# Optimization experiments

Hardware: AMD Instinct MI355X
Metric: run time of the kernel (lower is better)

The kernel has to match this reference:

```python
import jax, jax.numpy as jnp
import numpy as np
import math

DIM = 1024
CHUNK = 64
B, S = 4, 4096

def setup_inputs() -> dict:
    key = jax.random.key(0)
    ks = jax.random.split(key, 16)
    d = DIM
    std = 1.0 / math.sqrt(d)
    def lin(k):
        k1, k2 = jax.random.split(k)
        return (jax.random.uniform(k1, (d, d), jnp.float32, -std, std),
                jax.random.uniform(k2, (d,), jnp.float32, -std, std))
    Wk, bk = lin(ks[0])
    Wv, bv = lin(ks[1])
    Wq, bq = lin(ks[2])
    Wkp, bkp = lin(ks[3])
    Wqp, bqp = lin(ks[4])
    Wo, bo = lin(ks[5])
    return {
        "x": jax.random.normal(ks[6], (B, S, d), jnp.float32),
        "Wk": Wk, "bk": bk, "Wv": Wv, "bv": bv, "Wq": Wq, "bq": bq,
        "Wkp": Wkp, "bkp": bkp, "Wqp": Wqp, "bqp": bqp,
        "phase_scale": jnp.full((d,), math.pi, jnp.float32),
        "ln_g": jnp.ones((d,), jnp.float32),
        "ln_b": jnp.zeros((d,), jnp.float32),
        "Wo": Wo, "bo": bo,
    }

def _linear(x, W, b):
    # torch nn.Linear: x @ W.T + b
    return jnp.einsum('bsd,ed->bse', x, W) + b

def _layernorm(x, g, b, eps=1e-5):
    mu = jnp.mean(x, axis=-1, keepdims=True)
    var = jnp.var(x, axis=-1, keepdims=True)
    return (x - mu) * jax.lax.rsqrt(var + eps) * g + b

def reference(x, Wk, bk, Wv, bv, Wq, bq, Wkp, bkp, Wqp, bqp,
              phase_scale, ln_g, ln_b, Wo, bo):
    batch, seq_len, dim = x.shape
    key = _linear(x, Wk, bk)
    value = _linear(x, Wv, bv)
    query = _linear(x, Wq, bq)
    key_phase = jnp.tanh(_linear(key, Wkp, bkp)) * phase_scale
    query_phase = jnp.tanh(_linear(query, Wqp, bqp)) * phase_scale
    bound_real = value * jnp.cos(key_phase)
    bound_imag = value * jnpp_sin(key_phase) if False else value * jnp.sin(key_phase)
    pad_len = (CHUNK - seq_len % CHUNK) % CHUNK
    if pad_len > 0:
        pad = ((0, 0), (0, pad_len), (0, 0))
        bound_real = jnp.pad(bound_real, pad)
        bound_imag = jnp.pad(bound_imag, pad)
        query_phase = jnp.pad(query_phase, pad)
    padded_len = bound_real.shape[1]
    nc = padded_len // CHUNK
    br = bound_real.reshape(batch, nc, CHUNK, dim)
    bi = bound_imag.reshape(batch, nc, CHUNK, dim)
    qp = query_phase.reshape(batch, nc, CHUNK, dim)
    mem_real = jnp.cumsum(br, axis=2)
    mem_imag = jnp.cumsum(bi, axis=2)
    retrieved = mem_real * jnp.cos(qp) + mem_imag * jnp.sin(qp)
    retrieved = retrieved.reshape(batch, padded_len, dim)[:, :seq_len]
    retrieved = retrieved / math.sqrt(dim)
    out = _linear(_layernorm(retrieved, ln_g, ln_b), Wo, bo)
    return x + out
```

## Files before the change

### kernel.cpp

```cpp
#include <hip/hip_runtime.h>
#include <math.h>

#define DIMD 1024
#define CHUNKLEN 64
#define NTOK 16384

#define TM 128
#define TN 128
#define BK 64

typedef __bf16 bf16x8 __attribute__((ext_vector_type(8)));
typedef float floatx4 __attribute__((ext_vector_type(4)));
typedef unsigned short ushort8v __attribute__((ext_vector_type(8)));

__device__ __forceinline__ float bf2f(unsigned short u) {
  union { unsigned int i; float f; } v; v.i = ((unsigned int)u) << 16; return v.f;
}
__device__ __forceinline__ unsigned short f2bf(float f) {
  union { float f; unsigned int i; } v; v.f = f;
  unsigned int r = v.i + 0x7FFFu + ((v.i >> 16) & 1u);
  return (unsigned short)(r >> 16);
}

__device__ __forceinline__ float tanh_fast(float v) {
  const float t = __expf(2.0f * v);
  return 1.0f - 2.0f * __builtin_amdgcn_rcpf(t + 1.0f);
}

__device__ __forceinline__ void async16(const unsigned short* g, unsigned short* l) {
  __builtin_amdgcn_global_load_lds(
      (const __attribute__((address_space(1))) unsigned int*)g,
      (__attribute__((address_space(3))) unsigned int*)l, 16, 0, 0);
}

__global__ __launch_bounds__(256) void cvt_all_kernel(
    const float* __restrict__ x,
    const float* __restrict__ w0, const float* __restrict__ w1,
    const float* __restrict__ w2, const float* __restrict__ w3,
    unsigned short* __restrict__ dx,
    unsigned short* __restrict__ d0, unsigned short* __restrict__ d1,
    unsigned short* __restrict__ d2, unsigned short* __restrict__ d3)
{
  const int b = blockIdx.x;
  const float* src; unsigned short* dst; long i;
  if (b < 16384) {
    src = x; dst = dx; i = (long)b * 256 + threadIdx.x;
  } else {
    const int r = b - 16384;
    const int s = r >> 10;
    src = s == 0 ? w0 : s == 1 ? w1 : s == 2 ? w2 : w3;
    dst = s == 0 ? d0 : s == 1 ? d1 : s == 2 ? d2 : d3;
    i = (long)(r & 1023) * 256 + threadIdx.x;
  }
  const float4 v = ((const float4*)src)[i];
  ushort4 o;
  o.x = f2bf(v.x); o.y = f2bf(v.y); o.z = f2bf(v.z); o.w = f2bf(v.w);
  ((ushort4*)dst)[i] = o;
}

__global__ __launch_bounds__(256) void transpose_cvt_kernel(
    const float* __restrict__ s0, const float* __restrict__ s1,
    unsigned short* __restrict__ q0, unsigned short* __restrict__ q1)
{
  __shared__ unsigned short tile[64][66];
  const float* src = blockIdx.z ? s1 : s0;
  unsigned short* dst = blockIdx.z ? q1 : q0;
  const int e0 = blockIdx.y * 64;
  const int k0 = blockIdx.x * 64;
  const int t  = threadIdx.x;
  const int tr = t >> 4;
  const int tc = t & 15;
#pragma unroll
  for (int p = 0; p < 4; ++p) {
    const int el = p * 16 + tr;
    const float4 v = *(const float4*)&src[(long)(e0 + el) * DIMD + k0 + tc * 4];
    tile[el][tc * 4 + 0] = f2bf(v.x);
    tile[el][tc * 4 + 1] = f2bf(v.y);
    tile[el][tc * 4 + 2] = f2bf(v.z);
    tile[el][tc * 4 + 3] = f2bf(v.w);
  }
  __syncthreads();
#pragma unroll
  for (int p = 0; p < 4; ++p) {
    const int kl = p * 16 + tr;
    ushort4 o;
    o.x = tile[tc * 4 + 0][kl];
    o.y = tile[tc * 4 + 1][kl];
    o.z = tile[tc * 4 + 2][kl];
    o.w = tile[tc * 4 + 3][kl];
    *(ushort4*)&dst[(long)(k0 + kl) * DIMD + e0 + tc * 4] = o;
  }
}

__global__ __launch_bounds__(256) void bias_comb_kernel(
    const float* __restrict__ Wkp, const float* __restrict__ bk,
    const float* __restrict__ bkp,
    const float* __restrict__ Wqp, const float* __restrict__ bq,
    const float* __restrict__ bqp,
    float* __restrict__ bkq, float* __restrict__ bqq)
{
  const int b = blockIdx.x;
  const int which = b >> 8;
  const int lane = threadIdx.x & 63;
  const int wid  = threadIdx.x >> 6;
  const int n = (b & 255) * 4 + wid;
  const float* W    = which ? Wqp : Wkp;
  const float* bvec = which ? bq  : bk;
  const float* badd = which ? bqp : bkp;
  float*       outp = which ? bqq : bkq;
  float s = 0.f;
#pragma unroll
  for (int i = 0; i < 16; ++i)
    s += W[(long)n * DIMD + lane + i * 64] * bvec[lane + i * 64];
#pragma unroll
  for (int o = 32; o > 0; o >>= 1) s += __shfl_xor(s, o, 64);
  if (lane == 0) outp[n] = s + badd[n];
}

template <int MODE>
__global__ __launch_bounds__(256) void gemm_bt_kernel(
    const unsigned short* __restrict__ A0, const unsigned short* __restrict__ A1,
    const unsigned short* __restrict__ W0, const unsigned short* __restrict__ W1,
    const unsigned short* __restrict__ W2,
    const float* __restrict__ b0, const float* __restrict__ b1,
    const float* __restrict__ b2,
    const float* __restrict__ aux,
    unsigned short* __restrict__ O0, unsigned short* __restrict__ O1,
    unsigned short* __restrict__ O2,
    float* __restrict__ Of, const float* __restrict__ resid)
{
  __shared__ unsigned short lsA[TM * BK];
  __shared__ unsigned short lsB[TN * BK];

  const int tid  = threadIdx.x;
  const int lane = tid & 63;
  const int wid  = tid >> 6;
  const long bm  = (long)blockIdx.y * TM;
  const long bng = (long)blockIdx.x * TN;

  const unsigned short* A = A0;
  const unsigned short* W = W0;
  const float* bias = b0;
  unsigned short* Ob = O0;
  long bn = bng;
  int seg = 0;
  if (MODE == 0) {
    seg = (int)(bng >> 10);
    bn = bng & 1023;
    W    = seg == 0 ? W0 : (seg == 1 ? W1 : W2);
    bias = seg == 0 ? b0 : (seg == 1 ? b1 : b2);
    Ob   = seg == 0 ? O0 : (seg == 1 ? O1 : O2);
  } else if (MODE == 1) {
    if (blockIdx.z) { A = A1; W = W1; Ob = O1; }
  }

  const int wm = (wid & 1) * 64;
  const int wn = (wid >> 1) * 64;

  floatx4 acc[4][4];
#pragma unroll
  for (int i = 0; i < 4; ++i)
#pragma unroll
    for (int j = 0; j < 4; ++j)
      acc[i][j] = (floatx4)(0.0f);

  const int srow  = lane >> 3;
  const int pcol  = (lane & 7) * 8;
  const int lcolL = (((lane & 7) ^ (srow & 7)) * 8);
  const int frm   = lane & 15;
  const int cfrk  = lane >> 4;

  for (int kk = 0; kk < DIMD; kk += BK) {
    __syncthreads();
#pragma unroll
    for (int j = 0; j < 4; ++j) {
      const int inst = wid * 4 + j;
      const int r = inst * 8 + srow;
      async16(A + (bm + r) * (long)DIMD + kk + lcolL, &lsA[r * BK + pcol]);
      async16(W + (bn + r) * (long)DIMD + kk + lcolL, &lsB[r * BK + pcol]);
    }
    __syncthreads();
#pragma unroll
    for (int ks = 0; ks < BK; ks += 32) {
      const int cb  = (ks >> 3) + cfrk;
      const int swz = ((cb ^ (frm & 7)) << 3);
      bf16x8 af[4], bfr[4];
#pragma unroll
      for (int i = 0; i < 4; ++i)
        af[i]  = *(const bf16x8*)&lsA[(wm + i * 16 + frm) * BK + swz];
#pragma unroll
      for (int i = 0; i < 4; ++i)
        bfr[i] = *(const bf16x8*)&lsB[(wn + i * 16 + frm) * BK + swz];
#pragma unroll
      for (int i = 0; i < 4; ++i)
#pragma unroll
        for (int j = 0; j < 4; ++j)
          acc[i][j] = __builtin_amdgcn_mfma_f32_16x16x32_bf16(af[i], bfr[j], acc[i][j], 0, 0, 0);
    }
  }

  const int cn = lane & 15;
  const int rq = (lane >> 4) * 4;
#pragma unroll
  for (int j = 0; j < 4; ++j) {
    const long col = bn + wn + j * 16 + cn;
    const float bv = (MODE == 1) ? 0.0f : bias[col];
    const float pv = (MODE == 0) ? aux[col] : 0.0f;
#pragma unroll
    for (int i = 0; i < 4; ++i) {
#pragma unroll
      for (int r = 0; r < 4; ++r) {
        const long row = bm + wm + i * 16 + rq + r;
        const float v = acc[i][j][r] + bv;
        if (MODE == 0) {
          Ob[row * (long)DIMD + col] = (seg == 0) ? f2bf(v)
                                                  : f2bf(tanh_fast(v) * pv);
        } else if (MODE == 1) {
          Ob[row * (long)DIMD + col] = f2bf(v);
        } else {
          Of[row * (long)DIMD + col] = v + resid[row * (long)DIMD + col];
        }
      }
    }
  }
}

__global__ __launch_bounds__(512) void scan_ln_kernel(
    const unsigned short* __restrict__ V,  const unsigned short* __restrict__ KP,
    const unsigned short* __restrict__ QP,
    const float* __restrict__ lng, const float* __restrict__ lnb,
    unsigned short* __restrict__ out)
{
  __shared__ unsigned short ret_s[32][DIMD];

  const int tid  = threadIdx.x;
  const int lane = tid & 63;
  const int wid  = tid >> 6;
  const long rowBase = (long)blockIdx.x * CHUNKLEN;
  const int d0 = tid * 2;

  const int c0 = lane * 8;
  const int c1 = 512 + lane * 8;
  float g0[8], be0[8], g1[8], be1[8];
#pragma unroll
  for (int j = 0; j < 8; ++j) {
    g0[j] = lng[c0 + j]; be0[j] = lnb[c0 + j];
    g1[j] = lng[c1 + j]; be1[j] = lnb[c1 + j];
  }

  float mr[2] = {0.f, 0.f};
  float mi[2] = {0.f, 0.f};

  for (int h = 0; h < 2; ++h) {
    for (int tl = 0; tl < 32; ++tl) {
      const int t = h * 32 + tl;
      const long off = (rowBase + t) * DIMD + d0;
      const ushort2 v2 = *(const ushort2*)(V + off);
      const ushort2 k2 = *(const ushort2*)(KP + off);
      const ushort2 q2 = *(const ushort2*)(QP + off);
      const unsigned short va[2] = {v2.x, v2.y};
      const unsigned short ka[2] = {k2.x, k2.y};
      const unsigned short qa[2] = {q2.x, q2.y};
      unsigned short rv[2];
#pragma unroll
      for (int j = 0; j < 2; ++j) {
        const float v  = bf2f(va[j]);
        const float kp = bf2f(ka[j]);
        const float qp = bf2f(qa[j]);
        float skp, ckp, sqp, cqp;
        __sincosf(kp, &skp, &ckp);
        __sincosf(qp, &sqp, &cqp);
        mr[j] += v * ckp;
        mi[j] += v * skp;
        rv[j] = f2bf((mr[j] * cqp + mi[j] * sqp) * 0.03125f);
      }
      ushort2 o2; o2.x = rv[0]; o2.y = rv[1];
      *(ushort2*)&ret_s[tl][d0] = o2;
    }
    __syncthreads();

#pragma unroll 1
    for (int rr = 0; rr < 4; ++rr) {
      const int tl = wid * 4 + rr;
      const ushort8v a0 = *(const ushort8v*)&ret_s[tl][c0];
      const ushort8v a1 = *(const ushort8v*)&ret_s[tl][c1];
      float f0[8], f1[8];
      float s = 0.f, s2 = 0.f;
#pragma unroll
      for (int j = 0; j < 8; ++j) {
        f0[j] = bf2f(a0[j]); f1[j] = bf2f(a1[j]);
        s += f0[j] + f1[j];
        s2 += f0[j] * f0[j] + f1[j] * f1[j];
      }
#pragma unroll
      for (int o = 32; o > 0; o >>= 1) {
        s  += __shfl_xor(s,  o, 64);
        s2 += __shfl_xor(s2, o, 64);
      }
      const float mu  = s * (1.0f / DIMD);
      const float var = s2 * (1.0f / DIMD) - mu * mu;
      const float inv = rsqrtf(var + 1e-5f);
      ushort8v o0, o1;
#pragma unroll
      for (int j = 0; j < 8; ++j) {
        o0[j] = f2bf((f0[j] - mu) * inv * g0[j] + be0[j]);
        o1[j] = f2bf((f1[j] - mu) * inv * g1[j] + be1[j]);
      }
      const long gro = (rowBase + h * 32 + tl) * DIMD;
      *(ushort8v*)(out + gro + c0) = o0;
      *(ushort8v*)(out + gro + c1) = o1;
    }
    __syncthreads();
  }
}

extern "C" void kernel_launch(void* const* d_in, const int* in_sizes, int n_in,
                              void* d_out, int out_size, void* d_ws, size_t ws_size,
                              hipStream_t stream)
{
  const float* x   = (const float*)d_in[0];
  const float* Wk  = (const float*)d_in[1];
  const float* bk  = (const float*)d_in[2];
  const float* Wv  = (const float*)d_in[3];
  const float* bv  = (const float*)d_in[4];
  const float* Wq  = (const float*)d_in[5];
  const float* bq  = (const float*)d_in[6];
  const float* Wkp = (const float*)d_in[7];
  const float* bkp = (const float*)d_in[8];
  const float* Wqp = (const float*)d_in[9];
  const float* bqp = (const float*)d_in[10];
  const float* ph  = (const float*)d_in[11];
  const float* lng = (const float*)d_in[12];
  const float* lnb = (const float*)d_in[13];
  const float* Wo  = (const float*)d_in[14];
  const float* bo  = (const float*)d_in[15];
  float* out = (float*)d_out;

  const long NB = (long)NTOK * DIMD;
  const long DD = (long)DIMD * DIMD;
  const size_t required = (size_t)(4 * NB + 8 * DD) * sizeof(unsigned short)
                        + 2048 * sizeof(float);
  if (ws_size < required) return;

  unsigned short* S0   = (unsigned short*)d_ws;
  unsigned short* SV   = S0   + NB;
  unsigned short* SKP  = SV   + NB;
  unsigned short* SQP  = SKP  + NB;
  unsigned short* Wvb  = SQP  + NB;
  unsigned short* Wob  = Wvb  + DD;
  unsigned short* Wkpb = Wob  + DD;
  unsigned short* Wqpb = Wkpb + DD;
  unsigned short* WkT  = Wqpb + DD;
  unsigned short* WqT  = WkT  + DD;
  unsigned short* Wkqb = WqT  + DD;
  unsigned short* Wqqb = Wkqb + DD;
  float* bkq = (float*)(Wqqb + DD);
  float* bqq = bkq + DIMD;

  dim3 blk(256);

  cvt_all_kernel<<<dim3(16384 + 4 * 1024), blk, 0, stream>>>(
      x, Wv, Wo, Wkp, Wqp, S0, Wvb, Wob, Wkpb, Wqpb);
  transpose_cvt_kernel<<<dim3(16, 16, 2), blk, 0, stream>>>(Wk, Wq, WkT, WqT);
  bias_comb_kernel<<<dim3(512), blk, 0, stream>>>(Wkp, bk, bkp, Wqp, bq, bqp, bkq, bqq);
  gemm_bt_kernel<1><<<dim3(DIMD / TN, DIMD / TM, 2), blk, 0, stream>>>(
      Wkpb, Wqpb, WkT, WqT, nullptr, nullptr, nullptr, nullptr, nullptr,
      Wkqb, Wqqb, nullptr, nullptr, nullptr);
  gemm_bt_kernel<0><<<dim3(3 * DIMD / TN, NTOK / TM), blk, 0, stream>>>(
      S0, nullptr, Wvb, Wkqb, Wqqb, bv, bkq, bqq, ph, SV, SKP, SQP, nullptr, nullptr);
  scan_ln_kernel<<<dim3(NTOK / CHUNKLEN), dim3(512), 0, stream>>>(
      SV, SKP, SQP, lng, lnb, S0);
  gemm_bt_kernel<2><<<dim3(DIMD / TN, NTOK / TM), blk, 0, stream>>>(
      S0, nullptr, Wob, nullptr, nullptr, bo, nullptr, nullptr, nullptr,
      nullptr, nullptr, nullptr, out, x);
}
```

Measured before the change: 415.5 us.

## Replace main GEMMs with 256x256-tile, 512-thread double-buffered MFMA kernel

Adds a new GEMM kernel that uses 256x256 output tiles with 8 waves, each wave computing 128x64. It double-buffers A and B in LDS with async loads and interleaves half-K phases with barriers. It also uses an XOR-swizzled LDS layout, workgroup index swizzling for L2 locality, and raised wave priority around the MFMA bursts. The QKV projection GEMM and the output GEMM now use this kernel, which increases operand reuse and cuts global traffic per FLOP. The cost is a large LDS footprint and high register pressure, which can limit occupancy.

```diff
diff --git a/kernel.cpp b/kernel.cpp
--- a/kernel.cpp
+++ b/kernel.cpp
@@ -217,6 +217,163 @@
                                                   : f2bf(tanh_fast(v) * pv);
         } else if (MODE == 1) {
           Ob[row * (long)DIMD + col] = f2bf(v);
+        } else {
+          Of[row * (long)DIMD + col] = v + resid[row * (long)DIMD + col];
+        }
+      }
+    }
+  }
+}
+
+#define TILE16 16384
+#define HALF16 8192
+
+template <int MODE>
+__global__ __launch_bounds__(512, 2) void gemm256_kernel(
+    const unsigned short* __restrict__ A,
+    const unsigned short* __restrict__ W0, const unsigned short* __restrict__ W1,
+    const unsigned short* __restrict__ W2,
+    const float* __restrict__ b0, const float* __restrict__ b1,
+    const float* __restrict__ b2,
+    const float* __restrict__ aux,
+    unsigned short* __restrict__ O0, unsigned short* __restrict__ O1,
+    unsigned short* __restrict__ O2,
+    float* __restrict__ Of, const float* __restrict__ resid)
+{
+  __shared__ unsigned short lds[4 * TILE16];
+
+  const int tid  = threadIdx.x;
+  const int lane = tid & 63;
+  const int wid  = tid >> 6;
+
+  constexpr int NBX = (MODE == 0) ? 12 : 4;
+  constexpr int NWG = NBX * 64;
+  const int orig = blockIdx.x + blockIdx.y * gridDim.x;
+  const int swzb = (orig & 7) * (NWG >> 3) + (orig >> 3);
+  const int nb = swzb % NBX;
+  const int mb = swzb / NBX;
+
+  const long bm = (long)mb * 256;
+  long bn;
+  int seg = 0;
+  const unsigned short* W = W0;
+  const float* bias = b0;
+  unsigned short* Ob = O0;
+  if (MODE == 0) {
+    seg = nb >> 2;
+    bn  = (long)(nb & 3) * 256;
+    W    = seg == 0 ? W0 : (seg == 1 ? W1 : W2);
+    bias = seg == 0 ? b0 : (seg == 1 ? b1 : b2);
+    Ob   = seg == 0 ? O0 : (seg == 1 ? O1 : O2);
+  } else {
+    bn = (long)nb * 256;
+  }
+
+  const int wm = (wid >> 2) * 128;
+  const int wn = (wid & 3) * 64;
+
+  const int q0  = wid * 2;
+  const int sr0 = q0 * 16 + (lane >> 2);
+  const int sg  = (((lane & 3) ^ ((sr0 >> 1) & 3)) * 8);
+  const int sd0 = q0 * 512 + lane * 8;
+  const long arow = (bm + sr0) * (long)DIMD;
+  const long brow = (bn + sr0) * (long)DIMD;
+
+  const int frm   = lane & 15;
+  const int cfrk  = lane >> 4;
+  const int slot8 = (cfrk ^ ((frm >> 1) & 3)) * 8;
+  const int rbase = frm * 32 + slot8;
+
+  floatx4 acc[8][4];
+#pragma unroll
+  for (int i = 0; i < 8; ++i)
+#pragma unroll
+    for (int j = 0; j < 4; ++j) acc[i][j] = (floatx4)(0.0f);
+
+  bf16x8 bfr[4];
+
+#define SA256(buf, kk, h) do { \
+    const unsigned short* _s = A + arow + (kk) + (h) * 32 + sg; \
+    unsigned short* _d = &lds[(buf) * TILE16 + (h) * HALF16 + sd0]; \
+    async16(_s, _d); \
+    async16(_s + 16 * DIMD, _d + 512); \
+  } while (0)
+#define SB256(buf, kk, h) do { \
+    const unsigned short* _s = W + brow + (kk) + (h) * 32 + sg; \
+    unsigned short* _d = &lds[2 * TILE16 + (buf) * TILE16 + (h) * HALF16 + sd0]; \
+    async16(_s, _d); \
+    async16(_s + 16 * DIMD, _d + 512); \
+  } while (0)
+#define WAITBAR() do { \
+    asm volatile("s_waitcnt vmcnt(6)" ::: "memory"); \
+    __builtin_amdgcn_s_barrier(); \
+    asm volatile("" ::: "memory"); \
+    __builtin_amdgcn_sched_barrier(0); \
+  } while (0)
+#define BARC() do { \
+    asm volatile("" ::: "memory"); \
+    __builtin_amdgcn_s_barrier(); \
+    asm volatile("" ::: "memory"); \
+  } while (0)
+#define PHASE256(buf, h, ih, LOADB) do { \
+    bf16x8 af[4]; \
+    const int _ab = (buf) * TILE16 + (h) * HALF16 + (wm + (ih) * 64) * 32 + rbase; \
+    _Pragma("unroll") \
+    for (int i = 0; i < 4; ++i) af[i] = *(const bf16x8*)&lds[_ab + i * 512]; \
+    if (LOADB) { \
+      const int _bb = 2 * TILE16 + (buf) * TILE16 + (h) * HALF16 + wn * 32 + rbase; \
+      _Pragma("unroll") \
+      for (int j = 0; j < 4; ++j) bfr[j] = *(const bf16x8*)&lds[_bb + j * 512]; \
+    } \
+    __builtin_amdgcn_s_setprio(1); \
+    _Pragma("unroll") \
+    for (int i = 0; i < 4; ++i) \
+      _Pragma("unroll") \
+      for (int j = 0; j < 4; ++j) \
+        acc[(ih) * 4 + i][j] = __builtin_amdgcn_mfma_f32_16x16x32_bf16( \
+            af[i], bfr[j], acc[(ih) * 4 + i][j], 0, 0, 0); \
+    __builtin_amdgcn_s_setprio(0); \
+  } while (0)
+
+  SA256(0, 0, 0); SB256(0, 0, 0); SA256(0, 0, 1); SB256(0, 0, 1);
+
+#pragma unroll 1
+  for (int t = 0; t < 16; t += 2) {
+    const int k1 = (t + 1) * 64;
+    const int k2 = (t + 2 < 16) ? (t + 2) * 64 : 0;
+    SA256(1, k1, 0); WAITBAR(); PHASE256(0, 0, 0, true);  BARC();
+    SB256(1, k1, 0); BARC();    PHASE256(0, 0, 1, false); BARC();
+    SA256(1, k1, 1); WAITBAR(); PHASE256(0, 1, 0, true);  BARC();
+    SB256(1, k1, 1); BARC();    PHASE256(0, 1, 1, false); BARC();
+    SA256(0, k2, 0); WAITBAR(); PHASE256(1, 0, 0, true);  BARC();
+    SB256(0, k2, 0); BARC();    PHASE256(1, 0, 1, false); BARC();
+    SA256(0, k2, 1); WAITBAR(); PHASE256(1, 1, 0, true);  BARC();
+    SB256(0, k2, 1); BARC();    PHASE256(1, 1, 1, false); BARC();
+  }
+  asm volatile("s_waitcnt vmcnt(0)" ::: "memory");
+
+#undef SA256
+#undef SB256
+#undef WAITBAR
+#undef BARC
+#undef PHASE256
+
+  const int cn = lane & 15;
+  const int rq = (lane >> 4) * 4;
+#pragma unroll
+  for (int j = 0; j < 4; ++j) {
+    const long col = bn + wn + j * 16 + cn;
+    const float bv = bias[col];
+    const float pv = (MODE == 0) ? aux[col] : 0.0f;
+#pragma unroll
+    for (int ii = 0; ii < 8; ++ii) {
+#pragma unroll
+      for (int r = 0; r < 4; ++r) {
+        const long row = bm + wm + ii * 16 + rq + r;
+        const float v = acc[ii][j][r] + bv;
+        if (MODE == 0) {
+          Ob[row * (long)DIMD + col] = (seg == 0) ? f2bf(v)
+                                                  : f2bf(tanh_fast(v) * pv);
         } else {
           Of[row * (long)DIMD + col] = v + resid[row * (long)DIMD + col];
         }
@@ -366,11 +523,11 @@
   gemm_bt_kernel<1><<<dim3(DIMD / TN, DIMD / TM, 2), blk, 0, stream>>>(
       Wkpb, Wqpb, WkT, WqT, nullptr, nullptr, nullptr, nullptr, nullptr,
       Wkqb, Wqqb, nullptr, nullptr, nullptr);
-  gemm_bt_kernel<0><<<dim3(3 * DIMD / TN, NTOK / TM), blk, 0, stream>>>(
-      S0, nullptr, Wvb, Wkqb, Wqqb, bv, bkq, bqq, ph, SV, SKP, SQP, nullptr, nullptr);
+  gemm256_kernel<0><<<dim3(12, NTOK / 256), dim3(512), 0, stream>>>(
+      S0, Wvb, Wkqb, Wqqb, bv, bkq, bqq, ph, SV, SKP, SQP, nullptr, nullptr);
   scan_ln_kernel<<<dim3(NTOK / CHUNKLEN), dim3(512), 0, stream>>>(
       SV, SKP, SQP, lng, lnb, S0);
-  gemm_bt_kernel<2><<<dim3(DIMD / TN, NTOK / TM), blk, 0, stream>>>(
-      S0, nullptr, Wob, nullptr, nullptr, bo, nullptr, nullptr, nullptr,
+  gemm256_kernel<2><<<dim3(4, NTOK / 256), dim3(512), 0, stream>>>(
+      S0, Wob, nullptr, nullptr, bo, nullptr, nullptr, nullptr,
       nullptr, nullptr, nullptr, out, x);
 }
```

New measurement: 410.6 us. No clear change (-1.2%).
